# Optimization experiments

Measured on AMD Instinct MI355X. Metric: run time of the kernel, lower is better.

## Reference

```python
import jax, jax.numpy as jnp
import numpy as np

B, T, V, H, L = 2048, 128, 256, 20, 15  # batch, seq_len, vocab, hidden, max_label


def setup_inputs() -> dict:
    key = jax.random.key(0)
    ks = jax.random.split(key, 8)
    g = lambda k, shape, s: (jax.random.normal(k, shape, jnp.float32) * s)
    return {
        "x": jax.random.randint(ks[0], (B, T), 0, V, dtype=jnp.int32),
        "W0": g(ks[1], (V, 3 * H), 0.06),   # input kernel layer 0 [V, 3H] (z|r|h)
        "U0": g(ks[2], (H, 3 * H), 0.2),    # recurrent kernel layer 0
        "b0i": jnp.zeros((3 * H,), jnp.float32),  # input bias (reset_after=True split bias)
        "b0r": jnp.zeros((3 * H,), jnp.float32),  # recurrent bias
        "W1": g(ks[3], (H, 3 * H), 0.2),
        "U1": g(ks[4], (H, 3 * H), 0.2),
        "b1i": jnp.zeros((3 * H,), jnp.float32),
        "b1r": jnp.zeros((3 * H,), jnp.float32),
        "Wd": g(ks[5], (H, L), 0.2),
        "bd": jnp.zeros((L,), jnp.float32),
        "drop_rate": 0,  # identity dropout (deterministic reference)
    }


def _gru_cell(h, xw, U, br):
    # Keras GRUCell with reset_after=True:
    #   xw = x @ W + b_in  (precomputed), rec = h @ U + b_rec
    rec = h @ U + br
    xz, xr, xh = jnp.split(xw, 3, axis=-1)
    rz, rr, rh = jnp.split(rec, 3, axis=-1)
    z = jax.nn.sigmoid(xz + rz)
    r = jax.nn.sigmoid(xr + rr)
    hh = jnp.tanh(xh + r * rh)
    return z * h + (1.0 - z) * hh


def reference(x, W0, U0, b0i, b0r, W1, U1, b1i, b1r, Wd, bd, drop_rate):
    # one_hot(x) @ W0 == gather rows of W0 (same math, no [B,T,V] materialization)
    xW0 = W0[x] + b0i                 # [B, T, 3H]
    xW0 = jnp.swapaxes(xW0, 0, 1)     # [T, B, 3H] for scan over time

    def step(carry, xw_t):
        h0, h1 = carry
        h0 = _gru_cell(h0, xw_t, U0, b0r)
        xw1 = h0 @ W1 + b1i
        h1 = _gru_cell(h1, xw1, U1, b1r)
        return (h0, h1), None

    h0 = jnp.zeros((x.shape[0], H), W0.dtype)
    h1 = jnp.zeros((x.shape[0], H), W0.dtype)
    (h0, h1), _ = jax.lax.scan(step, (h0, h1), xW0)
    # tf.nn.dropout with rate 0 is the identity
    out = h1
    logits = jax.nn.softmax(out @ Wd + bd, axis=-1)  # [B, L]
    return logits
```

## Files before the change

kernel.cpp:

```cpp
#include <hip/hip_runtime.h>


#define BB 2048
#define TT 128
#define HH 20
#define LL 15
#define H3 60

typedef float v2f __attribute__((ext_vector_type(2)));

#if __has_builtin(__builtin_amdgcn_exp2f)
#define EXP2(x) __builtin_amdgcn_exp2f(x)
#else
#define EXP2(x) exp2f(x)
#endif

__device__ __forceinline__ float bclane(float v, int k) {
    return __int_as_float(__builtin_amdgcn_readlane(__float_as_int(v), k));
}
__device__ __forceinline__ float dpp_rshr1(float v) {
    return __int_as_float(__builtin_amdgcn_update_dpp(
        0, __float_as_int(v), 0x111, 0xF, 0xF, true));
}
__device__ __forceinline__ float dpp_rshr2(float v) {
    return __int_as_float(__builtin_amdgcn_update_dpp(
        0, __float_as_int(v), 0x112, 0xF, 0xF, true));
}
__device__ __forceinline__ float fast_rcp(float x) { return __builtin_amdgcn_rcpf(x); }

__device__ __forceinline__ void pk_fma(v2f& acc, v2f a, v2f b) {
    asm("v_pk_fma_f32 %0, %1, %2, %0" : "+v"(acc) : "v"(a), "v"(b));
}
__device__ __forceinline__ v2f pk_add(v2f a, v2f b) {
    v2f d;
    asm("v_pk_add_f32 %0, %1, %2" : "=v"(d) : "v"(a), "v"(b));
    return d;
}

#define PIN(v) asm volatile("" : "+v"(v))
#define LDSFENCE() asm volatile("" ::: "memory")

extern "C" __global__ __launch_bounds__(256)
__attribute__((amdgpu_waves_per_eu(2, 2)))
void gru2_kernel(const int* __restrict__ x, const float* __restrict__ W0,
                 const float* __restrict__ U0, const float* __restrict__ b0i,
                 const float* __restrict__ b0r, const float* __restrict__ W1,
                 const float* __restrict__ U1, const float* __restrict__ b1i,
                 const float* __restrict__ b1r, const float* __restrict__ Wd,
                 const float* __restrict__ bd, float* __restrict__ out)
{
    const int lane = threadIdx.x & 63;
    const int w = threadIdx.x >> 6;
    const int b = blockIdx.x * 4 + w;
    const int row = lane >> 4;
    const int pos = lane & 15;
    const int pc  = (pos < 15) ? pos : 14;
    const int u   = pc / 3;
    const int p3  = pc % 3;
    const int j   = row * 5 + u;
    const bool home = (pos < 15) && (p3 == 2);
    const int col = p3 * 20 + j;

    const float gsc = (p3 == 2) ? -2.8853900817779268f : -1.4426950408889634f;

    __shared__ __align__(16) float hbuf[4][2][24];
    float* h0buf = &hbuf[w][0][0];
    float* h1buf = &hbuf[w][1][0];
    const float4* h0q = (const float4*)h0buf;
    const float4* h1q = (const float4*)h1buf;
    if (home) { h0buf[j] = 0.f; h1buf[j] = 0.f; }
    LDSFENCE();

    v2f u0p[10], w1p[10], u1p[10];
#pragma unroll
    for (int q = 0; q < 10; ++q) {
        const int k0 = (2 * q) * H3, k1 = (2 * q + 1) * H3;
        u0p[q] = v2f{U0[k0 + col] * gsc, U0[k1 + col] * gsc};
        w1p[q] = v2f{W1[k0 + col] * gsc, W1[k1 + col] * gsc};
        u1p[q] = v2f{U1[k0 + col] * gsc, U1[k1 + col] * gsc};
    }
#pragma unroll
    for (int q = 0; q < 10; ++q) { PIN(u0p[q]); PIN(w1p[q]); PIN(u1p[q]); }
    float bi0 = b0i[col] * gsc, br0 = b0r[col] * gsc;
    float bi1 = b1i[col] * gsc, br1 = b1r[col] * gsc;
    PIN(bi0); PIN(br0); PIN(bi1); PIN(br1);

    const int* xrow = x + b * TT;
    const int tokA = xrow[lane];
    const int tokB = xrow[64 + lane];

    float h0 = 0.f, h1 = 0.f;

    const int tok0 = __builtin_amdgcn_readlane(tokA, 0);
    const int tok1 = __builtin_amdgcn_readlane(tokA, 1);
    int tokn2 = __builtin_amdgcn_readlane(tokA, 2);
    float xw_cur = fmaf(W0[tok0 * H3 + col], gsc, bi0);
    float xw_nxt = W0[tok1 * H3 + col];

    float4 c0[5], c1[5];
    float rec0, xw1, rec1;

#define DOT01()                                                               \
    {                                                                         \
        v2f a0a = v2f{br0, 0.f}, a0b = v2f{0.f, 0.f};                         \
        v2f a1a = v2f{bi1, 0.f}, a1b = v2f{0.f, 0.f};                         \
        _Pragma("unroll")                                                     \
        for (int q = 0; q < 5; ++q) {                                         \
            const v2f hA = v2f{c0[q].x, c0[q].y}, hB = v2f{c0[q].z, c0[q].w}; \
            pk_fma(a0a, hA, u0p[2 * q]);                                      \
            pk_fma(a0b, hB, u0p[2 * q + 1]);                                  \
            pk_fma(a1a, hA, w1p[2 * q]);                                      \
            pk_fma(a1b, hB, w1p[2 * q + 1]);                                  \
        }                                                                     \
        { const v2f t = pk_add(a0a, a0b); rec0 = t.x + t.y; }                 \
        { const v2f t = pk_add(a1a, a1b); xw1  = t.x + t.y; }                 \
    }
#define DOT2()                                                                \
    {                                                                         \
        v2f a2a = v2f{br1, 0.f}, a2b = v2f{0.f, 0.f};                         \
        _Pragma("unroll")                                                     \
        for (int q = 0; q < 5; ++q) {                                         \
            const v2f gA = v2f{c1[q].x, c1[q].y}, gB = v2f{c1[q].z, c1[q].w}; \
            pk_fma(a2a, gA, u1p[2 * q]);                                      \
            pk_fma(a2b, gB, u1p[2 * q + 1]);                                  \
        }                                                                     \
        { const v2f t = pk_add(a2a, a2b); rec1 = t.x + t.y; }                 \
    }
#define GATES(XW, REC, H)                                                     \
    {                                                                         \
        const float e_  = EXP2((XW) + (REC));                                 \
        const float t_  = fast_rcp(1.f + e_);                                 \
        const float rv_ = dpp_rshr1(t_);                                      \
        const float zv_ = dpp_rshr2(t_);                                      \
        const float eh_ = EXP2(fmaf(rv_, (REC), (XW)));                       \
        const float th_ = fast_rcp(1.f + eh_);                                \
        const float hh_ = fmaf(2.f, th_, -1.f);                               \
        H = fmaf(zv_, (H) - hh_, hh_);                                        \
    }

    {
        const float pf = W0[tokn2 * H3 + col];
        const int tokn3 = __builtin_amdgcn_readlane(tokA, 3);
        GATES(xw_cur, br0, h0);
        if (home) h0buf[j] = h0;
        LDSFENCE();
#pragma unroll
        for (int q = 0; q < 5; ++q) { c0[q] = h0q[q]; c1[q] = h1q[q]; }
        xw_cur = fmaf(xw_nxt, gsc, bi0); xw_nxt = pf; tokn2 = tokn3;
        DOT01();
    }

#pragma unroll 4
    for (int i = 1; i < TT; ++i) {
        const int t3 = (i + 3 < TT) ? (i + 3) : (TT - 1);
        const float pf = W0[tokn2 * H3 + col];
        const int tokn3 = __builtin_amdgcn_readlane(t3 < 64 ? tokA : tokB, t3 & 63);

        GATES(xw_cur, rec0, h0);
        if (home) h0buf[j] = h0;
        LDSFENCE();
#pragma unroll
        for (int q = 0; q < 5; ++q) c0[q] = h0q[q];

        DOT2();

        GATES(xw1, rec1, h1);
        if (home) h1buf[j] = h1;
        LDSFENCE();
#pragma unroll
        for (int q = 0; q < 5; ++q) c1[q] = h1q[q];

        xw_cur = fmaf(xw_nxt, gsc, bi0); xw_nxt = pf; tokn2 = tokn3;

        DOT01();
    }

    {
        DOT2();
        GATES(xw1, rec1, h1);
        if (home) h1buf[j] = h1;
        LDSFENCE();
    }

    const int l = lane < LL ? lane : LL - 1;
    float acc = bd[l];
#pragma unroll
    for (int k = 0; k < HH; ++k)
        acc = fmaf(h1buf[k], Wd[k * LL + l], acc);

    float m = acc;
#pragma unroll
    for (int i = 0; i < LL; ++i) m = fmaxf(m, bclane(acc, i));
    const float e = __expf(acc - m);
    float s = 0.f;
#pragma unroll
    for (int i = 0; i < LL; ++i) s += bclane(e, i);
    const float pr = e * fast_rcp(s);

    if (lane < LL) out[b * LL + lane] = pr;
}

extern "C" void kernel_launch(void* const* d_in, const int* in_sizes, int n_in,
                              void* d_out, int out_size, void* d_ws, size_t ws_size,
                              hipStream_t stream) {
    const int*   x   = (const int*)  d_in[0];
    const float* W0  = (const float*)d_in[1];
    const float* U0  = (const float*)d_in[2];
    const float* b0i = (const float*)d_in[3];
    const float* b0r = (const float*)d_in[4];
    const float* W1  = (const float*)d_in[5];
    const float* U1  = (const float*)d_in[6];
    const float* b1i = (const float*)d_in[7];
    const float* b1r = (const float*)d_in[8];
    const float* Wd  = (const float*)d_in[9];
    const float* bd  = (const float*)d_in[10];
    float* out = (float*)d_out;

    dim3 grid(BB / 4), block(256);
    hipLaunchKernelGGL(gru2_kernel, grid, block, 0, stream,
                       x, W0, U0, b0i, b0r, W1, U1, b1i, b1r, Wd, bd, out);
}
```

Measured before the change: 130.3 us.

## Broadcast hidden state via ds_bpermute instead of LDS store/load

Replaces the per-step LDS write of hidden state and vector reads with 20 ds_bpermute cross-lane reads per layer, removing the shared buffer. Packed FMA inline asm is replaced by scalar fmaf chains, and the loop unroll is reduced from 4 to 2. This aims to cut the store-to-load dependency through shared memory, but issues many more LDS-pipe instructions and uses more registers.

New measurement: 189.4 us. +45.3%, slower.

```diff
diff --git a/kernel.cpp b/kernel.cpp
--- a/kernel.cpp
+++ b/kernel.cpp
@@ -7,8 +7,6 @@
 #define LL 15
 #define H3 60
 
-typedef float v2f __attribute__((ext_vector_type(2)));
-
 #if __has_builtin(__builtin_amdgcn_exp2f)
 #define EXP2(x) __builtin_amdgcn_exp2f(x)
 #else
@@ -18,6 +16,9 @@
 __device__ __forceinline__ float bclane(float v, int k) {
     return __int_as_float(__builtin_amdgcn_readlane(__float_as_int(v), k));
 }
+__device__ __forceinline__ float bperm(int addr, float v) {
+    return __int_as_float(__builtin_amdgcn_ds_bpermute(addr, __float_as_int(v)));
+}
 __device__ __forceinline__ float dpp_rshr1(float v) {
     return __int_as_float(__builtin_amdgcn_update_dpp(
         0, __float_as_int(v), 0x111, 0xF, 0xF, true));
@@ -27,18 +28,7 @@
         0, __float_as_int(v), 0x112, 0xF, 0xF, true));
 }
 __device__ __forceinline__ float fast_rcp(float x) { return __builtin_amdgcn_rcpf(x); }
-
-__device__ __forceinline__ void pk_fma(v2f& acc, v2f a, v2f b) {
-    asm("v_pk_fma_f32 %0, %1, %2, %0" : "+v"(acc) : "v"(a), "v"(b));
-}
-__device__ __forceinline__ v2f pk_add(v2f a, v2f b) {
-    v2f d;
-    asm("v_pk_add_f32 %0, %1, %2" : "=v"(d) : "v"(a), "v"(b));
-    return d;
-}
-
 #define PIN(v) asm volatile("" : "+v"(v))
-#define LDSFENCE() asm volatile("" ::: "memory")
 
 extern "C" __global__ __launch_bounds__(256)
 __attribute__((amdgpu_waves_per_eu(2, 2)))
@@ -58,32 +48,29 @@
     const int u   = pc / 3;
     const int p3  = pc % 3;
     const int j   = row * 5 + u;
-    const bool home = (pos < 15) && (p3 == 2);
     const int col = p3 * 20 + j;
+    (void)j;
 
     const float gsc = (p3 == 2) ? -2.8853900817779268f : -1.4426950408889634f;
 
-    __shared__ __align__(16) float hbuf[4][2][24];
-    float* h0buf = &hbuf[w][0][0];
-    float* h1buf = &hbuf[w][1][0];
-    const float4* h0q = (const float4*)h0buf;
-    const float4* h1q = (const float4*)h1buf;
-    if (home) { h0buf[j] = 0.f; h1buf[j] = 0.f; }
-    LDSFENCE();
-
-    v2f u0p[10], w1p[10], u1p[10];
-#pragma unroll
-    for (int q = 0; q < 10; ++q) {
-        const int k0 = (2 * q) * H3, k1 = (2 * q + 1) * H3;
-        u0p[q] = v2f{U0[k0 + col] * gsc, U0[k1 + col] * gsc};
-        w1p[q] = v2f{W1[k0 + col] * gsc, W1[k1 + col] * gsc};
-        u1p[q] = v2f{U1[k0 + col] * gsc, U1[k1 + col] * gsc};
-    }
-#pragma unroll
-    for (int q = 0; q < 10; ++q) { PIN(u0p[q]); PIN(w1p[q]); PIN(u1p[q]); }
-    float bi0 = b0i[col] * gsc, br0 = b0r[col] * gsc;
-    float bi1 = b1i[col] * gsc, br1 = b1r[col] * gsc;
-    PIN(bi0); PIN(br0); PIN(bi1); PIN(br1);
+    int bpa[HH];
+#pragma unroll
+    for (int k = 0; k < HH; ++k)
+        bpa[k] = ((((k / 5) << 4) + (k % 5) * 3 + 2) << 2);
+#pragma unroll
+    for (int k = 0; k < HH; ++k) PIN(bpa[k]);
+
+    float u0c[HH], w1c[HH], u1c[HH];
+#pragma unroll
+    for (int k = 0; k < HH; ++k) {
+        u0c[k] = U0[k * H3 + col] * gsc;
+        w1c[k] = W1[k * H3 + col] * gsc;
+        u1c[k] = U1[k * H3 + col] * gsc;
+    }
+#pragma unroll
+    for (int k = 0; k < HH; ++k) { PIN(u0c[k]); PIN(w1c[k]); PIN(u1c[k]); }
+    const float bi0 = b0i[col] * gsc, br0 = b0r[col] * gsc;
+    const float bi1 = b1i[col] * gsc, br1 = b1r[col] * gsc;
 
     const int* xrow = x + b * TT;
     const int tokA = xrow[lane];
@@ -97,34 +84,36 @@
     float xw_cur = fmaf(W0[tok0 * H3 + col], gsc, bi0);
     float xw_nxt = W0[tok1 * H3 + col];
 
-    float4 c0[5], c1[5];
+    float bp0[HH], bp1[HH];
+#pragma unroll
+    for (int k = 0; k < HH; ++k) bp1[k] = 0.f;
     float rec0, xw1, rec1;
+
+#define BCAST(H, BP)                                                          \
+    _Pragma("unroll")                                                         \
+    for (int k = 0; k < HH; ++k) BP[k] = bperm(bpa[k], H);
 
 #define DOT01()                                                               \
     {                                                                         \
-        v2f a0a = v2f{br0, 0.f}, a0b = v2f{0.f, 0.f};                         \
-        v2f a1a = v2f{bi1, 0.f}, a1b = v2f{0.f, 0.f};                         \
+        float a0 = br0, e0 = 0.f, a1 = bi1, e1 = 0.f;                         \
         _Pragma("unroll")                                                     \
-        for (int q = 0; q < 5; ++q) {                                         \
-            const v2f hA = v2f{c0[q].x, c0[q].y}, hB = v2f{c0[q].z, c0[q].w}; \
-            pk_fma(a0a, hA, u0p[2 * q]);                                      \
-            pk_fma(a0b, hB, u0p[2 * q + 1]);                                  \
-            pk_fma(a1a, hA, w1p[2 * q]);                                      \
-            pk_fma(a1b, hB, w1p[2 * q + 1]);                                  \
+        for (int k = 0; k < HH / 2; ++k) {                                    \
+            a0 = fmaf(bp0[2 * k],     u0c[2 * k],     a0);                    \
+            e0 = fmaf(bp0[2 * k + 1], u0c[2 * k + 1], e0);                    \
+            a1 = fmaf(bp0[2 * k],     w1c[2 * k],     a1);                    \
+            e1 = fmaf(bp0[2 * k + 1], w1c[2 * k + 1], e1);                    \
         }                                                                     \
-        { const v2f t = pk_add(a0a, a0b); rec0 = t.x + t.y; }                 \
-        { const v2f t = pk_add(a1a, a1b); xw1  = t.x + t.y; }                 \
+        rec0 = a0 + e0; xw1 = a1 + e1;                                        \
     }
 #define DOT2()                                                                \
     {                                                                         \
-        v2f a2a = v2f{br1, 0.f}, a2b = v2f{0.f, 0.f};                         \
+        float a2 = br1, e2 = 0.f;                                             \
         _Pragma("unroll")                                                     \
-        for (int q = 0; q < 5; ++q) {                                         \
-            const v2f gA = v2f{c1[q].x, c1[q].y}, gB = v2f{c1[q].z, c1[q].w}; \
-            pk_fma(a2a, gA, u1p[2 * q]);                                      \
-            pk_fma(a2b, gB, u1p[2 * q + 1]);                                  \
+        for (int k = 0; k < HH / 2; ++k) {                                    \
+            a2 = fmaf(bp1[2 * k],     u1c[2 * k],     a2);                    \
+            e2 = fmaf(bp1[2 * k + 1], u1c[2 * k + 1], e2);                    \
         }                                                                     \
-        { const v2f t = pk_add(a2a, a2b); rec1 = t.x + t.y; }                 \
+        rec1 = a2 + e2;                                                       \
     }
 #define GATES(XW, REC, H)                                                     \
     {                                                                         \
@@ -142,33 +131,24 @@
         const float pf = W0[tokn2 * H3 + col];
         const int tokn3 = __builtin_amdgcn_readlane(tokA, 3);
         GATES(xw_cur, br0, h0);
-        if (home) h0buf[j] = h0;
-        LDSFENCE();
-#pragma unroll
-        for (int q = 0; q < 5; ++q) { c0[q] = h0q[q]; c1[q] = h1q[q]; }
+        BCAST(h0, bp0);
         xw_cur = fmaf(xw_nxt, gsc, bi0); xw_nxt = pf; tokn2 = tokn3;
         DOT01();
     }
 
-#pragma unroll 4
+#pragma unroll 2
     for (int i = 1; i < TT; ++i) {
         const int t3 = (i + 3 < TT) ? (i + 3) : (TT - 1);
         const float pf = W0[tokn2 * H3 + col];
         const int tokn3 = __builtin_amdgcn_readlane(t3 < 64 ? tokA : tokB, t3 & 63);
 
         GATES(xw_cur, rec0, h0);
-        if (home) h0buf[j] = h0;
-        LDSFENCE();
-#pragma unroll
-        for (int q = 0; q < 5; ++q) c0[q] = h0q[q];
+        BCAST(h0, bp0);
 
         DOT2();
 
         GATES(xw1, rec1, h1);
-        if (home) h1buf[j] = h1;
-        LDSFENCE();
-#pragma unroll
-        for (int q = 0; q < 5; ++q) c1[q] = h1q[q];
+        BCAST(h1, bp1);
 
         xw_cur = fmaf(xw_nxt, gsc, bi0); xw_nxt = pf; tokn2 = tokn3;
 
@@ -178,15 +158,14 @@
     {
         DOT2();
         GATES(xw1, rec1, h1);
-        if (home) h1buf[j] = h1;
-        LDSFENCE();
+        BCAST(h1, bp1);
     }
 
     const int l = lane < LL ? lane : LL - 1;
     float acc = bd[l];
 #pragma unroll
     for (int k = 0; k < HH; ++k)
-        acc = fmaf(h1buf[k], Wd[k * LL + l], acc);
+        acc = fmaf(bp1[k], Wd[k * LL + l], acc);
 
     float m = acc;
 #pragma unroll
```
